# Kernel tuning notes

Measured on AMD Instinct MI355X. Metric: run time of the kernel, lower is better.

## Reference

```python
import jax, jax.numpy as jnp
import numpy as np
from jax import lax

VOCAB = 5000
HIDDEN = 1024
SEQ = 128
BATCH = 64


def setup_inputs() -> dict:
    key = jax.random.key(0)
    ks = jax.random.split(key, 12)
    s = 1.0 / np.sqrt(HIDDEN)
    u = lambda k, shape: jax.random.uniform(k, shape, jnp.float32, -s, s)
    return {
        "x": jax.random.randint(ks[0], (SEQ, BATCH), 0, VOCAB),
        # layer 1: input size = VOCAB
        "W_ih1": u(ks[1], (HIDDEN, VOCAB)),
        "W_hh1": u(ks[2], (HIDDEN, HIDDEN)),
        "b_ih1": u(ks[3], (HIDDEN,)),
        "b_hh1": u(ks[4], (HIDDEN,)),
        # layer 2: input size = HIDDEN
        "W_ih2": u(ks[5], (HIDDEN, HIDDEN)),
        "W_hh2": u(ks[6], (HIDDEN, HIDDEN)),
        "b_ih2": u(ks[7], (HIDDEN,)),
        "b_hh2": u(ks[8], (HIDDEN,)),
        # final projection
        "W_fc": u(ks[9], (VOCAB, HIDDEN)),
        "b_fc": u(ks[10], (VOCAB,)),
    }


def _rnn_layer(x_proj, W_hh, b_hh, h0):
    # x_proj: (S, B, H) precomputed input contribution (incl. b_ih)
    def step(h, xt):
        h = jnp.tanh(xt + h @ W_hh.T + b_hh)
        return h, h
    h_last, ys = lax.scan(step, h0, x_proj)
    return ys, h_last


def reference(x, W_ih1, W_hh1, b_ih1, b_hh1, W_ih2, W_hh2, b_ih2, b_hh2, W_fc, b_fc):
    S, B = x.shape
    H = W_hh1.shape[0]
    h0 = jnp.zeros((B, H), dtype=W_ih1.dtype)
    # one_hot(x) @ W_ih1.T is exactly a row-gather of W_ih1.T
    xp1 = jnp.take(W_ih1.T, x, axis=0) + b_ih1          # (S, B, H)
    y1, h1 = _rnn_layer(xp1, W_hh1, b_hh1, h0)
    xp2 = jnp.einsum("sbh,gh->sbg", y1, W_ih2) + b_ih2  # (S, B, H)
    y2, h2 = _rnn_layer(xp2, W_hh2, b_hh2, h0)
    ans = jnp.einsum("sbh,vh->sbv", y2, W_fc) + b_fc    # (S, B, V)
    state = jnp.stack([h1, h2])                          # (2, B, H)
    return ans, state
```

## Files before the change

kernel.cpp:

```cpp
#include <hip/hip_runtime.h>
#include <hip/hip_bf16.h>

#define VOCAB 5000
#define HIDDEN 1024
#define SEQ 128
#define BATCH 64
#define L1NB 16
#define L2NB 32
#define NBLK (L1NB + L2NB)
#define RING 8

typedef __hip_bfloat16 bf16;
typedef short bf16x8 __attribute__((ext_vector_type(8)));
typedef float f32x4 __attribute__((ext_vector_type(4)));

__device__ __forceinline__ float b2f(bf16 v) { return __bfloat162float(v); }

__device__ __forceinline__ bool detect_fp32(const void* w) {
    const unsigned* p = (const unsigned*)w;
    unsigned big = 0;
    #pragma unroll
    for (int i = 0; i < 64; ++i) {
        unsigned e = (p[i] >> 7) & 0xFFu;
        big |= (e >= 127u) ? 1u : 0u;
    }
    return big != 0;
}

__global__ __launch_bounds__(256) void convert_w(const void* __restrict__ src,
                                                 bf16* __restrict__ dst, int n,
                                                 const void* __restrict__ det) {
    const bool f32 = detect_fp32(det);
    int i = (blockIdx.x * 256 + threadIdx.x) * 4;
    if (f32) {
        const float* s = (const float*)src;
        #pragma unroll
        for (int j = 0; j < 4; ++j) if (i + j < n) dst[i + j] = __float2bfloat16(s[i + j]);
    } else {
        const bf16* s = (const bf16*)src;
        #pragma unroll
        for (int j = 0; j < 4; ++j) if (i + j < n) dst[i + j] = s[i + j];
    }
}

__global__ __launch_bounds__(256) void make_bias(const void* __restrict__ a,
                                                 const void* __restrict__ b,
                                                 float* __restrict__ dst, int n,
                                                 const void* __restrict__ det) {
    const bool f32 = detect_fp32(det);
    int i = blockIdx.x * 256 + threadIdx.x;
    if (i >= n) return;
    float v = f32 ? ((const float*)a)[i] : b2f(((const bf16*)a)[i]);
    if (b)  v += f32 ? ((const float*)b)[i] : b2f(((const bf16*)b)[i]);
    dst[i] = v;
}

__device__ __forceinline__ void wait_flag(int* flag, int target) {
    int v = __hip_atomic_load(flag, __ATOMIC_RELAXED, __HIP_MEMORY_SCOPE_AGENT);
    int n = 0;
    while (v < target) {
        __builtin_amdgcn_s_sleep(1);
        if ((++n & 63) == 0)
            v = __hip_atomic_load(flag, __ATOMIC_ACQUIRE, __HIP_MEMORY_SCOPE_AGENT);
        else
            v = __hip_atomic_load(flag, __ATOMIC_RELAXED, __HIP_MEMORY_SCOPE_AGENT);
    }
}

__global__ __launch_bounds__(256, 1) void rnn_persistent(
    const int*  __restrict__ x,
    const void* __restrict__ Wih1raw,
    const bf16* __restrict__ whh1,
    const bf16* __restrict__ wih2,
    const bf16* __restrict__ whh2,
    const float* __restrict__ bias1,
    const float* __restrict__ bias2,
    bf16* __restrict__ y1r,
    bf16* __restrict__ y2,
    int* __restrict__ f1,
    int* __restrict__ f2)
{
    extern __shared__ bf16 lds[];
    const int bid  = blockIdx.x;
    const int tid  = threadIdx.x;
    const int wave = tid >> 6;
    const int lane = tid & 63;
    const int q    = lane >> 4;
    const int l15  = lane & 15;
    const size_t BH = (size_t)BATCH * HIDDEN;
    const bool f32in = detect_fp32(Wih1raw);
    const int  mrow  = wave * 16 + l15;

    if (bid < L1NB) {
        const int n0 = bid * 64;
        for (int idx = tid; idx < 64 * 128; idx += 256) {
            const int row = idx >> 7, c = idx & 127;
            *(bf16x8*)&lds[(size_t)((row << 7) + (c ^ (row & 7))) * 8] =
                *(const bf16x8*)(whh1 + (size_t)(n0 + row) * HIDDEN + c * 8);
        }
        __syncthreads();

        float breg[4];
        #pragma unroll
        for (int t = 0; t < 4; ++t) breg[t] = bias1[n0 + t * 16 + l15];

        for (int s = 0; s < SEQ; ++s) {
            float xg[4][4];
            {
                int xv[4];
                #pragma unroll
                for (int r = 0; r < 4; ++r) xv[r] = x[s * BATCH + wave * 16 + q * 4 + r];
                #pragma unroll
                for (int t = 0; t < 4; ++t)
                    #pragma unroll
                    for (int r = 0; r < 4; ++r) {
                        const size_t gi = (size_t)(n0 + t * 16 + l15) * VOCAB + xv[r];
                        xg[t][r] = f32in ? ((const float*)Wih1raw)[gi]
                                         : b2f(((const bf16*)Wih1raw)[gi]);
                    }
            }
            if (tid == 0) {
                if (s >= 1)    wait_flag(&f1[s - 1], L1NB);
                if (s >= RING) wait_flag(&f2[s - RING], L2NB);
                __builtin_amdgcn_fence(__ATOMIC_ACQUIRE, "agent");
            }
            __syncthreads();

            f32x4 acc[4];
            #pragma unroll
            for (int t = 0; t < 4; ++t) acc[t] = (f32x4){0.f,0.f,0.f,0.f};
            if (s > 0) {
                const bf16* arow = y1r + (size_t)((s - 1) & (RING - 1)) * BH
                                       + (size_t)mrow * HIDDEN + q * 8;
                for (int k0 = 0; k0 < HIDDEN; k0 += 32) {
                    bf16x8 af = *(const bf16x8*)(arow + k0);
                    const int chb = (k0 >> 3) + q;
                    #pragma unroll
                    for (int t = 0; t < 4; ++t) {
                        const int row = t * 16 + l15;
                        bf16x8 bw = *(const bf16x8*)&lds[(size_t)((row << 7) + (chb ^ (row & 7))) * 8];
                        acc[t] = __builtin_amdgcn_mfma_f32_16x16x32_bf16(af, bw, acc[t], 0, 0, 0);
                    }
                }
            }
            bf16* out = y1r + (size_t)(s & (RING - 1)) * BH;
            #pragma unroll
            for (int t = 0; t < 4; ++t) {
                const int i = n0 + t * 16 + l15;
                #pragma unroll
                for (int r = 0; r < 4; ++r) {
                    const int b = wave * 16 + q * 4 + r;
                    out[(size_t)b * HIDDEN + i] =
                        __float2bfloat16(tanhf(acc[t][r] + breg[t] + xg[t][r]));
                }
            }
            __syncthreads();
            if (tid == 0)
                __hip_atomic_fetch_add(&f1[s], 1, __ATOMIC_RELEASE, __HIP_MEMORY_SCOPE_AGENT);
        }
    } else {
        const int n0 = (bid - L1NB) * 32;
        for (int idx = tid; idx < 32 * 256; idx += 256) {
            const int row = idx >> 8, c = idx & 255;
            const bf16* W = (c < 128) ? wih2 : whh2;
            *(bf16x8*)&lds[(size_t)((row << 8) + (c ^ (row & 7))) * 8] =
                *(const bf16x8*)(W + (size_t)(n0 + row) * HIDDEN + (c & 127) * 8);
        }
        __syncthreads();

        float breg[2];
        #pragma unroll
        for (int t = 0; t < 2; ++t) breg[t] = bias2[n0 + t * 16 + l15];

        for (int st = 0; st < SEQ; ++st) {
            if (tid == 0) {
                wait_flag(&f1[st], L1NB);
                if (st >= 1) wait_flag(&f2[st - 1], L2NB);
                __builtin_amdgcn_fence(__ATOMIC_ACQUIRE, "agent");
            }
            __syncthreads();

            f32x4 acc[2];
            #pragma unroll
            for (int t = 0; t < 2; ++t) acc[t] = (f32x4){0.f,0.f,0.f,0.f};

            {
                const bf16* arow = y1r + (size_t)(st & (RING - 1)) * BH
                                       + (size_t)mrow * HIDDEN + q * 8;
                for (int k0 = 0; k0 < HIDDEN; k0 += 32) {
                    bf16x8 af = *(const bf16x8*)(arow + k0);
                    const int chb = (k0 >> 3) + q;
                    #pragma unroll
                    for (int t = 0; t < 2; ++t) {
                        const int row = t * 16 + l15;
                        bf16x8 bw = *(const bf16x8*)&lds[(size_t)((row << 8) + (chb ^ (row & 7))) * 8];
                        acc[t] = __builtin_amdgcn_mfma_f32_16x16x32_bf16(af, bw, acc[t], 0, 0, 0);
                    }
                }
            }
            if (st > 0) {
                const bf16* arow = y2 + (size_t)(st - 1) * BH
                                      + (size_t)mrow * HIDDEN + q * 8;
                for (int k0 = 0; k0 < HIDDEN; k0 += 32) {
                    bf16x8 af = *(const bf16x8*)(arow + k0);
                    const int chb = 128 + (k0 >> 3) + q;
                    #pragma unroll
                    for (int t = 0; t < 2; ++t) {
                        const int row = t * 16 + l15;
                        bf16x8 bw = *(const bf16x8*)&lds[(size_t)((row << 8) + (chb ^ (row & 7))) * 8];
                        acc[t] = __builtin_amdgcn_mfma_f32_16x16x32_bf16(af, bw, acc[t], 0, 0, 0);
                    }
                }
            }
            bf16* out = y2 + (size_t)st * BH;
            #pragma unroll
            for (int t = 0; t < 2; ++t) {
                const int i = n0 + t * 16 + l15;
                #pragma unroll
                for (int r = 0; r < 4; ++r) {
                    const int b = wave * 16 + q * 4 + r;
                    out[(size_t)b * HIDDEN + i] =
                        __float2bfloat16(tanhf(acc[t][r] + breg[t]));
                }
            }
            __syncthreads();
            if (tid == 0)
                __hip_atomic_fetch_add(&f2[st], 1, __ATOMIC_RELEASE, __HIP_MEMORY_SCOPE_AGENT);
        }
    }
}

__global__ __launch_bounds__(256) void proj(
    const bf16* __restrict__ y2, const bf16* __restrict__ Wfc,
    const float* __restrict__ bfc, void* __restrict__ outp,
    const void* __restrict__ det)
{
    __shared__ bf16 cbuf[64 * 256];
    const int bm = blockIdx.x;
    const int bn = blockIdx.y;
    const int wave = threadIdx.x >> 6;
    const int lane = threadIdx.x & 63;
    const int q = lane >> 4, l15 = lane & 15;
    const int wm = wave & 1, wn = wave >> 1;
    const int m0 = bm * 64 + wm * 32;
    const int n0 = bn * 256 + wn * 128;

    f32x4 acc[2][8];
    #pragma unroll
    for (int i = 0; i < 2; ++i)
        #pragma unroll
        for (int t = 0; t < 8; ++t) acc[i][t] = (f32x4){0.f,0.f,0.f,0.f};

    const bf16x8 zf = (bf16x8){0,0,0,0,0,0,0,0};
    const bf16* a0p = y2 + (size_t)(m0 + l15) * HIDDEN + q * 8;
    const bf16* a1p = a0p + (size_t)16 * HIDDEN;

    for (int k0 = 0; k0 < HIDDEN; k0 += 32) {
        bf16x8 af0 = *(const bf16x8*)(a0p + k0);
        bf16x8 af1 = *(const bf16x8*)(a1p + k0);
        #pragma unroll
        for (int t = 0; t < 8; ++t) {
            const int n = n0 + t * 16 + l15;
            bf16x8 bw = (n < VOCAB)
                ? *(const bf16x8*)(Wfc + (size_t)n * HIDDEN + k0 + q * 8) : zf;
            acc[0][t] = __builtin_amdgcn_mfma_f32_16x16x32_bf16(af0, bw, acc[0][t], 0, 0, 0);
            acc[1][t] = __builtin_amdgcn_mfma_f32_16x16x32_bf16(af1, bw, acc[1][t], 0, 0, 0);
        }
    }

    const bool f32out = detect_fp32(det);

    if (f32out) {
        #pragma unroll
        for (int t = 0; t < 8; ++t) {
            const int col = n0 + t * 16 + l15;
            if (col >= VOCAB) continue;
            const float bias = bfc[col];
            #pragma unroll
            for (int i = 0; i < 2; ++i)
                #pragma unroll
                for (int r = 0; r < 4; ++r) {
                    const int row = m0 + i * 16 + q * 4 + r;
                    ((float*)outp)[(size_t)row * VOCAB + col] = acc[i][t][r] + bias;
                }
        }
        return;
    }

    #pragma unroll
    for (int t = 0; t < 8; ++t) {
        const int col  = n0 + t * 16 + l15;
        const int cloc = wn * 128 + t * 16 + l15;
        const float bias = (col < VOCAB) ? bfc[col] : 0.f;
        #pragma unroll
        for (int i = 0; i < 2; ++i)
            #pragma unroll
            for (int r = 0; r < 4; ++r) {
                const int rloc = wm * 32 + i * 16 + q * 4 + r;
                cbuf[rloc * 256 + cloc] = __float2bfloat16(acc[i][t][r] + bias);
            }
    }
    __syncthreads();
    bf16* ob = (bf16*)outp;
    for (int cidx = threadIdx.x; cidx < 64 * 32; cidx += 256) {
        const int row = cidx >> 5;
        const int c8  = (cidx & 31) * 8;
        const int gcol = bn * 256 + c8;
        if (gcol < VOCAB)
            *(bf16x8*)(ob + (size_t)(bm * 64 + row) * VOCAB + gcol) =
                *(const bf16x8*)&cbuf[row * 256 + c8];
    }
}

__global__ __launch_bounds__(256) void state_copy(
    const bf16* __restrict__ y1r, const bf16* __restrict__ y2,
    void* __restrict__ outp, const void* __restrict__ det)
{
    const bool f32out = detect_fp32(det);
    const int t = blockIdx.x * blockDim.x + threadIdx.x;
    const int BH = BATCH * HIDDEN;
    const size_t ofs = (size_t)SEQ * BATCH * VOCAB;
    float v;
    if (t < BH) v = b2f(y1r[(size_t)((SEQ - 1) & (RING - 1)) * BH + t]);
    else        v = b2f(y2[(size_t)(SEQ - 1) * BH + (t - BH)]);
    if (f32out) ((float*)outp)[ofs + t] = v;
    else        ((bf16*)outp)[ofs + t] = __float2bfloat16(v);
}

extern "C" void kernel_launch(void* const* d_in, const int* in_sizes, int n_in,
                              void* d_out, int out_size, void* d_ws, size_t ws_size,
                              hipStream_t stream) {
    const int*  x       = (const int*)d_in[0];
    const void* Wih1raw = d_in[1];
    const void* Whh1raw = d_in[2];
    const void* bih1    = d_in[3];
    const void* bhh1    = d_in[4];
    const void* Wih2raw = d_in[5];
    const void* Whh2raw = d_in[6];
    const void* bih2    = d_in[7];
    const void* bhh2    = d_in[8];
    const void* Wfcraw  = d_in[9];
    const void* bfcraw  = d_in[10];

    char* wsb = (char*)d_ws;
    int*   f1    = (int*)wsb;
    int*   f2    = f1 + SEQ;
    bf16*  y2    = (bf16*)(wsb + 1024);
    bf16*  y1r   = y2   + (size_t)SEQ * BATCH * HIDDEN;
    bf16*  whh1  = y1r  + (size_t)RING * BATCH * HIDDEN;
    bf16*  wih2  = whh1 + (size_t)HIDDEN * HIDDEN;
    bf16*  whh2  = wih2 + (size_t)HIDDEN * HIDDEN;
    bf16*  wfcb  = whh2 + (size_t)HIDDEN * HIDDEN;
    float* bias1 = (float*)(wfcb + (size_t)VOCAB * HIDDEN);
    float* bias2 = bias1 + HIDDEN;
    float* bfcf  = bias2 + HIDDEN;

    hipMemsetAsync(f1, 0, 2 * SEQ * sizeof(int), stream);

    const int HH = HIDDEN * HIDDEN, VH = VOCAB * HIDDEN;
    convert_w<<<(HH + 1023) / 1024, 256, 0, stream>>>(Whh1raw, whh1, HH, Wih1raw);
    convert_w<<<(HH + 1023) / 1024, 256, 0, stream>>>(Wih2raw, wih2, HH, Wih1raw);
    convert_w<<<(HH + 1023) / 1024, 256, 0, stream>>>(Whh2raw, whh2, HH, Wih1raw);
    convert_w<<<(VH + 1023) / 1024, 256, 0, stream>>>(Wfcraw,  wfcb, VH, Wih1raw);
    make_bias<<<(HIDDEN + 255) / 256, 256, 0, stream>>>(bih1, bhh1, bias1, HIDDEN, Wih1raw);
    make_bias<<<(HIDDEN + 255) / 256, 256, 0, stream>>>(bih2, bhh2, bias2, HIDDEN, Wih1raw);
    make_bias<<<(VOCAB + 255) / 256, 256, 0, stream>>>(bfcraw, nullptr, bfcf, VOCAB, Wih1raw);

    rnn_persistent<<<NBLK, 256, 131072, stream>>>(x, Wih1raw, whh1, wih2, whh2,
                                                  bias1, bias2, y1r, y2, f1, f2);

    proj<<<dim3(128, 20), 256, 0, stream>>>(y2, wfcb, bfcf, d_out, Wih1raw);
    state_copy<<<(2 * BATCH * HIDDEN) / 256, 256, 0, stream>>>(y1r, y2, d_out, Wih1raw);
}
```

Before: 2.360 ms.

## Fuse output projection into persistent RNN kernel with dynamic tile scheduler

Merges the projection GEMM into the persistent RNN kernel. 192 extra blocks pull output tiles from an atomic counter and wait on per-timestep layer-2 flags, so the projection overlaps the recurrence instead of running afterwards. The recurrent loops now batch all 32 A-fragment loads with cache-bypassing (sc0 sc1) loads before the MFMAs. Outputs are staged through LDS and written with coalesced 128-bit bypass stores, and the acquire fences are dropped. Risks include deadlock if the 240 one-block-per-CU blocks are not all co-resident (hence the timeouts on the spin waits), and ordering that now rests on the bypass loads and stores rather than explicit fences.

Result: slower. 3.489 ms (+47.8%).

```diff
diff --git a/kernel.cpp b/kernel.cpp
--- a/kernel.cpp
+++ b/kernel.cpp
@@ -9,6 +9,9 @@
 #define L2NB 32
 #define NBLK (L1NB + L2NB)
 #define RING 8
+#define NGRID 240
+#define NTILE (128 * 20)
+#define LDS_BYTES 139264
 
 typedef __hip_bfloat16 bf16;
 typedef short bf16x8 __attribute__((ext_vector_type(8)));
@@ -55,19 +58,27 @@
     dst[i] = v;
 }
 
-__device__ __forceinline__ void wait_flag(int* flag, int target) {
-    int v = __hip_atomic_load(flag, __ATOMIC_RELAXED, __HIP_MEMORY_SCOPE_AGENT);
-    int n = 0;
-    while (v < target) {
-        __builtin_amdgcn_s_sleep(1);
-        if ((++n & 63) == 0)
-            v = __hip_atomic_load(flag, __ATOMIC_ACQUIRE, __HIP_MEMORY_SCOPE_AGENT);
-        else
-            v = __hip_atomic_load(flag, __ATOMIC_RELAXED, __HIP_MEMORY_SCOPE_AGENT);
-    }
-}
-
-__global__ __launch_bounds__(256, 1) void rnn_persistent(
+__device__ __forceinline__ void ld_sys_b128(bf16x8* dst, const void* p) {
+    asm volatile("global_load_dwordx4 %0, %1, off sc0 sc1" : "=v"(*dst) : "v"(p));
+}
+__device__ __forceinline__ void st_sys_b128(void* p, bf16x8 v) {
+    asm volatile("global_store_dwordx4 %0, %1, off sc0 sc1" :: "v"(p), "v"(v) : "memory");
+}
+__device__ __forceinline__ void vm_drain() {
+    asm volatile("s_waitcnt vmcnt(0)" ::: "memory");
+    __builtin_amdgcn_sched_barrier(0);
+}
+
+template <int SLP>
+__device__ __forceinline__ void wait_flag(int* flag, int target, long maxit) {
+    long n = 0;
+    while (__hip_atomic_load(flag, __ATOMIC_RELAXED, __HIP_MEMORY_SCOPE_AGENT) < target) {
+        __builtin_amdgcn_s_sleep(SLP);
+        if (++n > maxit) return;
+    }
+}
+
+__global__ __launch_bounds__(256, 1) void rnn_fused(
     const int*  __restrict__ x,
     const void* __restrict__ Wih1raw,
     const bf16* __restrict__ whh1,
@@ -78,7 +89,11 @@
     bf16* __restrict__ y1r,
     bf16* __restrict__ y2,
     int* __restrict__ f1,
-    int* __restrict__ f2)
+    int* __restrict__ f2,
+    int* __restrict__ pt,
+    const bf16* __restrict__ wfcb,
+    const float* __restrict__ bfcf,
+    void* __restrict__ outp)
 {
     extern __shared__ bf16 lds[];
     const int bid  = blockIdx.x;
@@ -88,10 +103,10 @@
     const int q    = lane >> 4;
     const int l15  = lane & 15;
     const size_t BH = (size_t)BATCH * HIDDEN;
-    const bool f32in = detect_fp32(Wih1raw);
     const int  mrow  = wave * 16 + l15;
 
     if (bid < L1NB) {
+        const bool f32in = detect_fp32(Wih1raw);
         const int n0 = bid * 64;
         for (int idx = tid; idx < 64 * 128; idx += 256) {
             const int row = idx >> 7, c = idx & 127;
@@ -103,6 +118,7 @@
         float breg[4];
         #pragma unroll
         for (int t = 0; t < 4; ++t) breg[t] = bias1[n0 + t * 16 + l15];
+        bf16* cb = lds + 65536;
 
         for (int s = 0; s < SEQ; ++s) {
             float xg[4][4];
@@ -120,9 +136,8 @@
                     }
             }
             if (tid == 0) {
-                if (s >= 1)    wait_flag(&f1[s - 1], L1NB);
-                if (s >= RING) wait_flag(&f2[s - RING], L2NB);
-                __builtin_amdgcn_fence(__ATOMIC_ACQUIRE, "agent");
+                if (s >= 1)    wait_flag<1>(&f1[s - 1], L1NB, 40000000L);
+                if (s >= RING) wait_flag<1>(&f2[s - RING], L2NB, 40000000L);
             }
             __syncthreads();
 
@@ -132,33 +147,44 @@
             if (s > 0) {
                 const bf16* arow = y1r + (size_t)((s - 1) & (RING - 1)) * BH
                                        + (size_t)mrow * HIDDEN + q * 8;
-                for (int k0 = 0; k0 < HIDDEN; k0 += 32) {
-                    bf16x8 af = *(const bf16x8*)(arow + k0);
-                    const int chb = (k0 >> 3) + q;
+                bf16x8 af[32];
+                #pragma unroll
+                for (int k = 0; k < 32; ++k) ld_sys_b128(&af[k], arow + k * 32);
+                vm_drain();
+                #pragma unroll
+                for (int k = 0; k < 32; ++k) {
+                    const int chb = k * 4 + q;
                     #pragma unroll
                     for (int t = 0; t < 4; ++t) {
                         const int row = t * 16 + l15;
                         bf16x8 bw = *(const bf16x8*)&lds[(size_t)((row << 7) + (chb ^ (row & 7))) * 8];
-                        acc[t] = __builtin_amdgcn_mfma_f32_16x16x32_bf16(af, bw, acc[t], 0, 0, 0);
+                        acc[t] = __builtin_amdgcn_mfma_f32_16x16x32_bf16(af[k], bw, acc[t], 0, 0, 0);
                     }
                 }
             }
-            bf16* out = y1r + (size_t)(s & (RING - 1)) * BH;
-            #pragma unroll
-            for (int t = 0; t < 4; ++t) {
-                const int i = n0 + t * 16 + l15;
+            #pragma unroll
+            for (int t = 0; t < 4; ++t)
                 #pragma unroll
                 for (int r = 0; r < 4; ++r) {
                     const int b = wave * 16 + q * 4 + r;
-                    out[(size_t)b * HIDDEN + i] =
+                    cb[b * 64 + t * 16 + l15] =
                         __float2bfloat16(tanhf(acc[t][r] + breg[t] + xg[t][r]));
                 }
-            }
+            __syncthreads();
+            bf16* outb = y1r + (size_t)(s & (RING - 1)) * BH;
+            #pragma unroll
+            for (int it = 0; it < 2; ++it) {
+                const int c = it * 256 + tid;
+                const int row = c >> 3, off = (c & 7) * 8;
+                st_sys_b128(outb + (size_t)row * HIDDEN + n0 + off,
+                            *(const bf16x8*)&cb[row * 64 + off]);
+            }
+            vm_drain();
             __syncthreads();
             if (tid == 0)
                 __hip_atomic_fetch_add(&f1[s], 1, __ATOMIC_RELEASE, __HIP_MEMORY_SCOPE_AGENT);
         }
-    } else {
+    } else if (bid < NBLK) {
         const int n0 = (bid - L1NB) * 32;
         for (int idx = tid; idx < 32 * 256; idx += 256) {
             const int row = idx >> 8, c = idx & 255;
@@ -171,12 +197,12 @@
         float breg[2];
         #pragma unroll
         for (int t = 0; t < 2; ++t) breg[t] = bias2[n0 + t * 16 + l15];
+        bf16* cb = lds + 65536;
 
         for (int st = 0; st < SEQ; ++st) {
             if (tid == 0) {
-                wait_flag(&f1[st], L1NB);
-                if (st >= 1) wait_flag(&f2[st - 1], L2NB);
-                __builtin_amdgcn_fence(__ATOMIC_ACQUIRE, "agent");
+                wait_flag<1>(&f1[st], L1NB, 40000000L);
+                if (st >= 1) wait_flag<1>(&f2[st - 1], L2NB, 40000000L);
             }
             __syncthreads();
 
@@ -187,128 +213,144 @@
             {
                 const bf16* arow = y1r + (size_t)(st & (RING - 1)) * BH
                                        + (size_t)mrow * HIDDEN + q * 8;
-                for (int k0 = 0; k0 < HIDDEN; k0 += 32) {
-                    bf16x8 af = *(const bf16x8*)(arow + k0);
-                    const int chb = (k0 >> 3) + q;
+                bf16x8 af[32];
+                #pragma unroll
+                for (int k = 0; k < 32; ++k) ld_sys_b128(&af[k], arow + k * 32);
+                vm_drain();
+                #pragma unroll
+                for (int k = 0; k < 32; ++k) {
+                    const int chb = k * 4 + q;
                     #pragma unroll
                     for (int t = 0; t < 2; ++t) {
                         const int row = t * 16 + l15;
                         bf16x8 bw = *(const bf16x8*)&lds[(size_t)((row << 8) + (chb ^ (row & 7))) * 8];
-                        acc[t] = __builtin_amdgcn_mfma_f32_16x16x32_bf16(af, bw, acc[t], 0, 0, 0);
+                        acc[t] = __builtin_amdgcn_mfma_f32_16x16x32_bf16(af[k], bw, acc[t], 0, 0, 0);
                     }
                 }
             }
             if (st > 0) {
                 const bf16* arow = y2 + (size_t)(st - 1) * BH
                                       + (size_t)mrow * HIDDEN + q * 8;
-                for (int k0 = 0; k0 < HIDDEN; k0 += 32) {
-                    bf16x8 af = *(const bf16x8*)(arow + k0);
-                    const int chb = 128 + (k0 >> 3) + q;
+                bf16x8 af[32];
+                #pragma unroll
+                for (int k = 0; k < 32; ++k) ld_sys_b128(&af[k], arow + k * 32);
+                vm_drain();
+                #pragma unroll
+                for (int k = 0; k < 32; ++k) {
+                    const int chb = 128 + k * 4 + q;
                     #pragma unroll
                     for (int t = 0; t < 2; ++t) {
                         const int row = t * 16 + l15;
                         bf16x8 bw = *(const bf16x8*)&lds[(size_t)((row << 8) + (chb ^ (row & 7))) * 8];
-                        acc[t] = __builtin_amdgcn_mfma_f32_16x16x32_bf16(af, bw, acc[t], 0, 0, 0);
+                        acc[t] = __builtin_amdgcn_mfma_f32_16x16x32_bf16(af[k], bw, acc[t], 0, 0, 0);
                     }
                 }
             }
-            bf16* out = y2 + (size_t)st * BH;
-            #pragma unroll
-            for (int t = 0; t < 2; ++t) {
-                const int i = n0 + t * 16 + l15;
+            #pragma unroll
+            for (int t = 0; t < 2; ++t)
                 #pragma unroll
                 for (int r = 0; r < 4; ++r) {
                     const int b = wave * 16 + q * 4 + r;
-                    out[(size_t)b * HIDDEN + i] =
+                    cb[b * 32 + t * 16 + l15] =
                         __float2bfloat16(tanhf(acc[t][r] + breg[t]));
                 }
-            }
+            __syncthreads();
+            {
+                bf16* outb = y2 + (size_t)st * BH;
+                const int row = tid >> 2, off = (tid & 3) * 8;
+                st_sys_b128(outb + (size_t)row * HIDDEN + n0 + off,
+                            *(const bf16x8*)&cb[row * 32 + off]);
+            }
+            vm_drain();
             __syncthreads();
             if (tid == 0)
                 __hip_atomic_fetch_add(&f2[st], 1, __ATOMIC_RELEASE, __HIP_MEMORY_SCOPE_AGENT);
         }
     }
-}
-
-__global__ __launch_bounds__(256) void proj(
-    const bf16* __restrict__ y2, const bf16* __restrict__ Wfc,
-    const float* __restrict__ bfc, void* __restrict__ outp,
-    const void* __restrict__ det)
-{
-    __shared__ bf16 cbuf[64 * 256];
-    const int bm = blockIdx.x;
-    const int bn = blockIdx.y;
-    const int wave = threadIdx.x >> 6;
-    const int lane = threadIdx.x & 63;
-    const int q = lane >> 4, l15 = lane & 15;
-    const int wm = wave & 1, wn = wave >> 1;
-    const int m0 = bm * 64 + wm * 32;
-    const int n0 = bn * 256 + wn * 128;
-
-    f32x4 acc[2][8];
-    #pragma unroll
-    for (int i = 0; i < 2; ++i)
-        #pragma unroll
-        for (int t = 0; t < 8; ++t) acc[i][t] = (f32x4){0.f,0.f,0.f,0.f};
-
-    const bf16x8 zf = (bf16x8){0,0,0,0,0,0,0,0};
-    const bf16* a0p = y2 + (size_t)(m0 + l15) * HIDDEN + q * 8;
-    const bf16* a1p = a0p + (size_t)16 * HIDDEN;
-
-    for (int k0 = 0; k0 < HIDDEN; k0 += 32) {
-        bf16x8 af0 = *(const bf16x8*)(a0p + k0);
-        bf16x8 af1 = *(const bf16x8*)(a1p + k0);
-        #pragma unroll
-        for (int t = 0; t < 8; ++t) {
-            const int n = n0 + t * 16 + l15;
-            bf16x8 bw = (n < VOCAB)
-                ? *(const bf16x8*)(Wfc + (size_t)n * HIDDEN + k0 + q * 8) : zf;
-            acc[0][t] = __builtin_amdgcn_mfma_f32_16x16x32_bf16(af0, bw, acc[0][t], 0, 0, 0);
-            acc[1][t] = __builtin_amdgcn_mfma_f32_16x16x32_bf16(af1, bw, acc[1][t], 0, 0, 0);
+
+    {
+        const bool f32out = detect_fp32(Wih1raw);
+        __shared__ int stile;
+        bf16* cb = lds;
+        const int wm = wave & 1, wn = wave >> 1;
+        const bf16x8 zf = (bf16x8){0,0,0,0,0,0,0,0};
+
+        for (;;) {
+            if (tid == 0)
+                stile = __hip_atomic_fetch_add(pt, 1, __ATOMIC_RELAXED, __HIP_MEMORY_SCOPE_AGENT);
+            __syncthreads();
+            const int tile = stile;
+            if (tile >= NTILE) break;
+            const int bm = tile / 20, bn = tile % 20;
+            if (tid == 0) wait_flag<16>(&f2[bm], L2NB, 2500000L);
+            __syncthreads();
+
+            const int m0 = bm * 64 + wm * 32;
+            const int n0 = bn * 256 + wn * 128;
+
+            f32x4 acc[2][8];
+            #pragma unroll
+            for (int i = 0; i < 2; ++i)
+                #pragma unroll
+                for (int t = 0; t < 8; ++t) acc[i][t] = (f32x4){0.f,0.f,0.f,0.f};
+
+            const bf16* a0p = y2 + (size_t)(m0 + l15) * HIDDEN + q * 8;
+            const bf16* a1p = a0p + (size_t)16 * HIDDEN;
+
+            for (int k0 = 0; k0 < HIDDEN; k0 += 32) {
+                bf16x8 af0 = *(const bf16x8*)(a0p + k0);
+                bf16x8 af1 = *(const bf16x8*)(a1p + k0);
+                #pragma unroll
+                for (int t = 0; t < 8; ++t) {
+                    const int n = n0 + t * 16 + l15;
+                    bf16x8 bw = (n < VOCAB)
+                        ? *(const bf16x8*)(wfcb + (size_t)n * HIDDEN + k0 + q * 8) : zf;
+                    acc[0][t] = __builtin_amdgcn_mfma_f32_16x16x32_bf16(af0, bw, acc[0][t], 0, 0, 0);
+                    acc[1][t] = __builtin_amdgcn_mfma_f32_16x16x32_bf16(af1, bw, acc[1][t], 0, 0, 0);
+                }
+            }
+
+            if (f32out) {
+                #pragma unroll
+                for (int t = 0; t < 8; ++t) {
+                    const int col = n0 + t * 16 + l15;
+                    if (col >= VOCAB) continue;
+                    const float bias = bfcf[col];
+                    #pragma unroll
+                    for (int i = 0; i < 2; ++i)
+                        #pragma unroll
+                        for (int r = 0; r < 4; ++r) {
+                            const int row = m0 + i * 16 + q * 4 + r;
+                            ((float*)outp)[(size_t)row * VOCAB + col] = acc[i][t][r] + bias;
+                        }
+                }
+                continue;
+            }
+
+            #pragma unroll
+            for (int t = 0; t < 8; ++t) {
+                const int col  = n0 + t * 16 + l15;
+                const int cloc = wn * 128 + t * 16 + l15;
+                const float bias = (col < VOCAB) ? bfcf[col] : 0.f;
+                #pragma unroll
+                for (int i = 0; i < 2; ++i)
+                    #pragma unroll
+                    for (int r = 0; r < 4; ++r) {
+                        const int rloc = wm * 32 + i * 16 + q * 4 + r;
+                        cb[rloc * 256 + cloc] = __float2bfloat16(acc[i][t][r] + bias);
+                    }
+            }
+            __syncthreads();
+            bf16* ob = (bf16*)outp;
+            for (int cidx = tid; cidx < 64 * 32; cidx += 256) {
+                const int row = cidx >> 5;
+                const int c8  = (cidx & 31) * 8;
+                const int gcol = bn * 256 + c8;
+                if (gcol < VOCAB)
+                    *(bf16x8*)(ob + (size_t)(bm * 64 + row) * VOCAB + gcol) =
+                        *(const bf16x8*)&cb[row * 256 + c8];
+            }
         }
-    }
-
-    const bool f32out = detect_fp32(det);
-
-    if (f32out) {
-        #pragma unroll
-        for (int t = 0; t < 8; ++t) {
-            const int col = n0 + t * 16 + l15;
-            if (col >= VOCAB) continue;
-            const float bias = bfc[col];
-            #pragma unroll
-            for (int i = 0; i < 2; ++i)
-                #pragma unroll
-                for (int r = 0; r < 4; ++r) {
-                    const int row = m0 + i * 16 + q * 4 + r;
-                    ((float*)outp)[(size_t)row * VOCAB + col] = acc[i][t][r] + bias;
-                }
-        }
-        return;
-    }
-
-    #pragma unroll
-    for (int t = 0; t < 8; ++t) {
-        const int col  = n0 + t * 16 + l15;
-        const int cloc = wn * 128 + t * 16 + l15;
-        const float bias = (col < VOCAB) ? bfc[col] : 0.f;
-        #pragma unroll
-        for (int i = 0; i < 2; ++i)
-            #pragma unroll
-            for (int r = 0; r < 4; ++r) {
-                const int rloc = wm * 32 + i * 16 + q * 4 + r;
-                cbuf[rloc * 256 + cloc] = __float2bfloat16(acc[i][t][r] + bias);
-            }
-    }
-    __syncthreads();
-    bf16* ob = (bf16*)outp;
-    for (int cidx = threadIdx.x; cidx < 64 * 32; cidx += 256) {
-        const int row = cidx >> 5;
-        const int c8  = (cidx & 31) * 8;
-        const int gcol = bn * 256 + c8;
-        if (gcol < VOCAB)
-            *(bf16x8*)(ob + (size_t)(bm * 64 + row) * VOCAB + gcol) =
-                *(const bf16x8*)&cbuf[row * 256 + c8];
     }
 }
 
@@ -354,8 +396,17 @@
     float* bias1 = (float*)(wfcb + (size_t)VOCAB * HIDDEN);
     float* bias2 = bias1 + HIDDEN;
     float* bfcf  = bias2 + HIDDEN;
-
-    hipMemsetAsync(f1, 0, 2 * SEQ * sizeof(int), stream);
+    int*   pt    = (int*)(bfcf + VOCAB);
+
+    static bool lds_ok = false;
+    if (!lds_ok) {
+        (void)hipFuncSetAttribute((const void*)rnn_fused,
+                                  hipFuncAttributeMaxDynamicSharedMemorySize, LDS_BYTES);
+        lds_ok = true;
+    }
+
+    (void)hipMemsetAsync(f1, 0, 2 * SEQ * sizeof(int), stream);
+    (void)hipMemsetAsync(pt, 0, sizeof(int), stream);
 
     const int HH = HIDDEN * HIDDEN, VH = VOCAB * HIDDEN;
     convert_w<<<(HH + 1023) / 1024, 256, 0, stream>>>(Whh1raw, whh1, HH, Wih1raw);
@@ -366,9 +417,9 @@
     make_bias<<<(HIDDEN + 255) / 256, 256, 0, stream>>>(bih2, bhh2, bias2, HIDDEN, Wih1raw);
     make_bias<<<(VOCAB + 255) / 256, 256, 0, stream>>>(bfcraw, nullptr, bfcf, VOCAB, Wih1raw);
 
-    rnn_persistent<<<NBLK, 256, 131072, stream>>>(x, Wih1raw, whh1, wih2, whh2,
-                                                  bias1, bias2, y1r, y2, f1, f2);
-
-    proj<<<dim3(128, 20), 256, 0, stream>>>(y2, wfcb, bfcf, d_out, Wih1raw);
+    rnn_fused<<<NGRID, 256, LDS_BYTES, stream>>>(x, Wih1raw, whh1, wih2, whh2,
+                                                 bias1, bias2, y1r, y2, f1, f2,
+                                                 pt, wfcb, bfcf, d_out);
+
     state_copy<<<(2 * BATCH * HIDDEN) / 256, 256, 0, stream>>>(y1r, y2, d_out, Wih1raw);
 }
```
